# Performance work log

Measured on AMD Instinct MI355X. Metric: run time of the kernel, lower is better.

Reference implementation:

```python
import jax, jax.numpy as jnp
import numpy as np

B, H, W, C = 32, 64, 64, 256


def setup_inputs() -> dict:
    key = jax.random.key(0)
    ks = jax.random.split(key, 4)
    scale = 1.0 / np.sqrt(C)
    return {
        "x": jax.random.normal(ks[0], (B, H, W, C), dtype=jnp.float32),
        "wq": jax.random.normal(ks[1], (C, C), dtype=jnp.float32) * scale,
        "bq": jnp.zeros((C,), dtype=jnp.float32),
        "wk": jax.random.normal(ks[2], (C, C), dtype=jnp.float32) * scale,
        "bk": jnp.zeros((C,), dtype=jnp.float32),
        "wv": jax.random.normal(ks[3], (C, C), dtype=jnp.float32) * scale,
        "bv": jnp.zeros((C,), dtype=jnp.float32),
    }


def reference(x, wq, bq, wk, bk, wv, bv):
    # 1x1 convs == per-pixel dense projections
    q = jnp.einsum('bhwc,cf->bhwf', x, wq) + bq
    k = jnp.einsum('bhwc,cf->bhwf', x, wk) + bk
    v = jnp.einsum('bhwc,cf->bhwf', x, wv) + bv
    # tf.matmul(key, query, transpose_b=True): batch dims (b,h), contract over c
    attn = jnp.einsum('bhwc,bhvc->bhwv', k, q)  # [B,H,W,W], NO 1/sqrt(d) scaling
    attn = jax.nn.softmax(attn, axis=-1)
    out = jnp.einsum('bhwv,bhvc->bhwc', attn, v)  # [B,H,W,C]
    return out * x  # elementwise gate with raw input
```

## Files before the change

### kernel.cpp

```cpp
#include <hip/hip_runtime.h>

#define CD   256
#define WD   64
#define NBH  2048
#define XST  264
#define VST  72
#define SST  68

typedef unsigned short u16;
typedef __attribute__((ext_vector_type(8))) short bfrag_t;
typedef __attribute__((ext_vector_type(4))) float f4_t;

#define MFMA(a, b, c) __builtin_amdgcn_mfma_f32_16x16x32_bf16(a, b, c, 0, 0, 0)

__device__ __forceinline__ u16 f2bf(float f) {
    unsigned u = __float_as_uint(f);
    u += 0x7fffu + ((u >> 16) & 1u);
    return (u16)(u >> 16);
}
__device__ __forceinline__ float bf2f(u16 h) {
    return __uint_as_float(((unsigned)h) << 16);
}

__global__ __launch_bounds__(256) void prep_all(
    const float* __restrict__ wq, const float* __restrict__ wk,
    const float* __restrict__ wv, const float* __restrict__ bk,
    u16* __restrict__ Mthi, u16* __restrict__ Mtlo,
    u16* __restrict__ Wvthi, float* __restrict__ wqbk)
{
    __shared__ float smem[12336];
    const int t = threadIdx.x;
    const int b = blockIdx.x;

    if (b < 128) {
        float* swq = smem;
        float* swk = smem + 16 * 257;
        const int dt = b >> 3;
        const int ct = b & 7;
        #pragma unroll
        for (int n = 0; n < 16; ++n) {
            int idx = n * 256 + t;
            int d = idx >> 8, f = idx & 255;
            swq[d * 257 + f] = wq[(dt * 16 + d) * CD + f];
        }
        #pragma unroll
        for (int n = 0; n < 32; ++n) {
            int idx = n * 256 + t;
            int c = idx >> 8, f = idx & 255;
            swk[c * 257 + f] = wk[(ct * 32 + c) * CD + f];
        }
        __syncthreads();
        const int d = t & 15, c0 = (t >> 4) * 2;
        #pragma unroll
        for (int cc = 0; cc < 2; ++cc) {
            const float* kr = &swk[(c0 + cc) * 257];
            const float* qr = &swq[d * 257];
            float acc = 0.f;
            #pragma unroll 8
            for (int f = 0; f < CD; ++f) acc = fmaf(kr[f], qr[f], acc);
            u16 h = f2bf(acc);
            int off = (dt * 16 + d) * CD + ct * 32 + c0 + cc;
            Mthi[off] = h;
            Mtlo[off] = f2bf(acc - bf2f(h));
        }
    } else if (b < 144) {
        float* tile = smem;
        const int bb = b - 128;
        const int bc = bb >> 2, bd = bb & 3;
        #pragma unroll
        for (int n = 0; n < 16; ++n) {
            int idx = n * 256 + t;
            int c = idx >> 6, d = idx & 63;
            tile[c * 65 + d] = wv[(bc * 64 + c) * CD + bd * 64 + d];
        }
        __syncthreads();
        #pragma unroll
        for (int n = 0; n < 16; ++n) {
            int idx = n * 256 + t;
            int d = idx >> 6, c = idx & 63;
            Wvthi[(bd * 64 + d) * CD + bc * 64 + c] = f2bf(tile[c * 65 + d]);
        }
    } else {
        float* sbk = smem;
        if (t < CD) sbk[t] = bk[t];
        __syncthreads();
        const int c = (b - 144) * 16 + (t >> 4), part = t & 15;
        const float* wr = wq + c * CD + part * 16;
        const float* br = sbk + part * 16;
        float a = 0.f;
        #pragma unroll
        for (int j = 0; j < 16; ++j) a = fmaf(wr[j], br[j], a);
        a += __shfl_xor(a, 1);
        a += __shfl_xor(a, 2);
        a += __shfl_xor(a, 4);
        a += __shfl_xor(a, 8);
        if (part == 0) wqbk[c] = a;
    }
}

extern __shared__ char smem_raw[];

__global__ __launch_bounds__(1024, 4) void attn_kernel(
    const float* __restrict__ x,
    const u16* __restrict__ Mthi, const u16* __restrict__ Mtlo,
    const u16* __restrict__ Wvthi, const float* __restrict__ wqbk,
    const float* __restrict__ bv, float* __restrict__ out)
{
    u16* sXhi = (u16*)smem_raw;
    u16* sXlo = sXhi + WD * XST;
    u16* sThi = sXlo + WD * XST;
    u16* sTlo = sThi + WD * XST;
    u16* sVt  = sThi;
    float* sS  = (float*)(sTlo + WD * XST);
    float* sxb = sS + WD * SST;
    float* sbv = sxb + WD;

    const int t = threadIdx.x;
    const int wave = t >> 6, lane = t & 63;
    const int lane15 = lane & 15, quad = lane >> 4;
    const int bh = blockIdx.x;
    const float* __restrict__ xblk = x + (size_t)bh * (WD * CD);
    float* __restrict__ oblk = out + (size_t)bh * (WD * CD);

    if (t < CD) sbv[t] = bv[t];
    {
        const float4* xv4 = (const float4*)xblk;
        #pragma unroll
        for (int n = 0; n < 4; ++n) {
            int idx = n * 1024 + t;
            float4 v = xv4[idx];
            int i = idx >> 6;
            int c = (idx & 63) << 2;
            ushort4 h4, l4;
            h4.x = f2bf(v.x); l4.x = f2bf(v.x - bf2f(h4.x));
            h4.y = f2bf(v.y); l4.y = f2bf(v.y - bf2f(h4.y));
            h4.z = f2bf(v.z); l4.z = f2bf(v.z - bf2f(h4.z));
            h4.w = f2bf(v.w); l4.w = f2bf(v.w - bf2f(h4.w));
            *(ushort4*)&sXhi[i * XST + c] = h4;
            *(ushort4*)&sXlo[i * XST + c] = l4;
        }
    }
    {
        const int row = t >> 4, part = t & 15;
        const float* xr = xblk + row * CD + part * 16;
        const float* br = wqbk + part * 16;
        float a = 0.f;
        #pragma unroll
        for (int i = 0; i < 4; ++i) {
            float4 xv = *(const float4*)&xr[i * 4];
            float4 bvv = *(const float4*)&br[i * 4];
            a = fmaf(xv.x, bvv.x, a); a = fmaf(xv.y, bvv.y, a);
            a = fmaf(xv.z, bvv.z, a); a = fmaf(xv.w, bvv.w, a);
        }
        a += __shfl_xor(a, 1);
        a += __shfl_xor(a, 2);
        a += __shfl_xor(a, 4);
        a += __shfl_xor(a, 8);
        if (part == 0) sxb[row] = a;
    }
    __syncthreads();

    {
        f4_t acc[4];
        const f4_t z = {0.f, 0.f, 0.f, 0.f};
        #pragma unroll
        for (int a = 0; a < 4; ++a) acc[a] = z;

        const int drow = wave * 16 + lane15;
        const u16* mh = Mthi + drow * CD + quad * 8;
        const u16* ml = Mtlo + drow * CD + quad * 8;
        bfrag_t Ah[8], Al[8];
        #pragma unroll
        for (int kk = 0; kk < 8; ++kk) {
            Ah[kk] = *(const bfrag_t*)(mh + kk * 32);
            Al[kk] = *(const bfrag_t*)(ml + kk * 32);
        }
        #pragma unroll
        for (int kk = 0; kk < 8; ++kk) {
            const int k0 = kk * 32 + quad * 8;
            bfrag_t Bh[4], Bl[4];
            #pragma unroll
            for (int nt = 0; nt < 4; ++nt) {
                const int xo = (nt * 16 + lane15) * XST + k0;
                Bh[nt] = *(const bfrag_t*)(sXhi + xo);
                Bl[nt] = *(const bfrag_t*)(sXlo + xo);
            }
            #pragma unroll
            for (int nt = 0; nt < 4; ++nt) {
                acc[nt] = MFMA(Ah[kk], Bh[nt], acc[nt]);
                acc[nt] = MFMA(Ah[kk], Bl[nt], acc[nt]);
                acc[nt] = MFMA(Al[kk], Bh[nt], acc[nt]);
            }
        }
        #pragma unroll
        for (int nt = 0; nt < 4; ++nt) {
            const int i  = nt * 16 + lane15;
            const int d0 = wave * 16 + quad * 4;
            ushort4 h4, l4;
            float f;
            f = acc[nt][0]; h4.x = f2bf(f); l4.x = f2bf(f - bf2f(h4.x));
            f = acc[nt][1]; h4.y = f2bf(f); l4.y = f2bf(f - bf2f(h4.y));
            f = acc[nt][2]; h4.z = f2bf(f); l4.z = f2bf(f - bf2f(h4.z));
            f = acc[nt][3]; h4.w = f2bf(f); l4.w = f2bf(f - bf2f(h4.w));
            *(ushort4*)&sThi[i * XST + d0] = h4;
            *(ushort4*)&sTlo[i * XST + d0] = l4;
        }
    }
    __syncthreads();

    {
        const f4_t z = {0.f, 0.f, 0.f, 0.f};
        f4_t a0 = z, a1 = z, a2 = z;
        const int m0 = (wave >> 2) * 16;
        const int n0 = (wave & 3) * 16;
        #pragma unroll
        for (int kk = 0; kk < 8; ++kk) {
            const int k0 = kk * 32 + quad * 8;
            const int to = (m0 + lane15) * XST + k0;
            const int xo = (n0 + lane15) * XST + k0;
            bfrag_t Th = *(const bfrag_t*)(sThi + to);
            bfrag_t Tl = *(const bfrag_t*)(sTlo + to);
            bfrag_t Xh = *(const bfrag_t*)(sXhi + xo);
            bfrag_t Xl = *(const bfrag_t*)(sXlo + xo);
            a0 = MFMA(Th, Xh, a0);
            a1 = MFMA(Th, Xl, a1);
            a2 = MFMA(Tl, Xh, a2);
        }
        const int v = n0 + lane15;
        const float xbv = sxb[v];
        #pragma unroll
        for (int r = 0; r < 4; ++r) {
            const int wtok = m0 + quad * 4 + r;
            sS[wtok * SST + v] = a0[r] + a1[r] + a2[r] + xbv;
        }
    }
    __syncthreads();

    {
        f4_t acc[4];
        const f4_t z = {0.f, 0.f, 0.f, 0.f};
        #pragma unroll
        for (int a = 0; a < 4; ++a) acc[a] = z;

        const int drow = wave * 16 + lane15;
        const u16* wvp = Wvthi + drow * CD + quad * 8;
        bfrag_t Av[8];
        #pragma unroll
        for (int kk = 0; kk < 8; ++kk)
            Av[kk] = *(const bfrag_t*)(wvp + kk * 32);
        #pragma unroll
        for (int kk = 0; kk < 8; ++kk) {
            const int k0 = kk * 32 + quad * 8;
            #pragma unroll
            for (int nt = 0; nt < 4; ++nt) {
                bfrag_t Bf = *(const bfrag_t*)(sXhi + (nt * 16 + lane15) * XST + k0);
                acc[nt] = MFMA(Av[kk], Bf, acc[nt]);
            }
        }
        #pragma unroll
        for (int nt = 0; nt < 4; ++nt) {
            const int j = nt * 16 + lane15;
            #pragma unroll
            for (int r = 0; r < 4; ++r) {
                const int d = wave * 16 + quad * 4 + r;
                sVt[d * VST + j] = f2bf(acc[nt][r] + sbv[d]);
            }
        }
    }
    {
        const int row = t >> 4, part = t & 15;
        float* srow = &sS[row * SST + part * 4];
        float e[4];
        float mx = fmaxf(fmaxf(srow[0], srow[1]), fmaxf(srow[2], srow[3]));
        mx = fmaxf(mx, __shfl_xor(mx, 1));
        mx = fmaxf(mx, __shfl_xor(mx, 2));
        mx = fmaxf(mx, __shfl_xor(mx, 4));
        mx = fmaxf(mx, __shfl_xor(mx, 8));
        float sum = 0.f;
        #pragma unroll
        for (int u = 0; u < 4; ++u) { e[u] = __expf(srow[u] - mx); sum += e[u]; }
        sum += __shfl_xor(sum, 1);
        sum += __shfl_xor(sum, 2);
        sum += __shfl_xor(sum, 4);
        sum += __shfl_xor(sum, 8);
        float inv = 1.0f / sum;
        #pragma unroll
        for (int u = 0; u < 4; ++u) srow[u] = e[u] * inv;
    }
    __syncthreads();

    {
        f4_t acc[4];
        const f4_t z = {0.f, 0.f, 0.f, 0.f};
        #pragma unroll
        for (int a = 0; a < 4; ++a) acc[a] = z;

        const int m0 = (wave & 3) * 16;
        const int nbase = (wave >> 2) * 64;
        #pragma unroll
        for (int kk = 0; kk < 2; ++kk) {
            const int k0 = kk * 32 + quad * 8;
            const float* p = &sS[(m0 + lane15) * SST + k0];
            f4_t p0 = *(const f4_t*)p;
            f4_t p1 = *(const f4_t*)(p + 4);
            bfrag_t Af;
            Af[0] = (short)f2bf(p0[0]); Af[1] = (short)f2bf(p0[1]);
            Af[2] = (short)f2bf(p0[2]); Af[3] = (short)f2bf(p0[3]);
            Af[4] = (short)f2bf(p1[0]); Af[5] = (short)f2bf(p1[1]);
            Af[6] = (short)f2bf(p1[2]); Af[7] = (short)f2bf(p1[3]);
            #pragma unroll
            for (int nt = 0; nt < 4; ++nt) {
                bfrag_t Bf = *(const bfrag_t*)(sVt + (nbase + nt * 16 + lane15) * VST + k0);
                acc[nt] = MFMA(Af, Bf, acc[nt]);
            }
        }
        #pragma unroll
        for (int nt = 0; nt < 4; ++nt) {
            const int d = nbase + nt * 16 + lane15;
            #pragma unroll
            for (int r = 0; r < 4; ++r) {
                const int wtok = m0 + quad * 4 + r;
                float g = xblk[wtok * CD + d];
                oblk[wtok * CD + d] = acc[nt][r] * g;
            }
        }
    }
}

extern "C" void kernel_launch(void* const* d_in, const int* in_sizes, int n_in,
                              void* d_out, int out_size, void* d_ws, size_t ws_size,
                              hipStream_t stream) {
    const float* x  = (const float*)d_in[0];
    const float* wq = (const float*)d_in[1];
    const float* wk = (const float*)d_in[3];
    const float* bk = (const float*)d_in[4];
    const float* wv = (const float*)d_in[5];
    const float* bv = (const float*)d_in[6];
    float* out = (float*)d_out;

    char* ws = (char*)d_ws;
    u16* Mthi   = (u16*)ws;
    u16* Mtlo   = (u16*)(ws + (128 << 10));
    u16* Wvthi  = (u16*)(ws + (256 << 10));
    float* wqbk = (float*)(ws + (384 << 10));

    prep_all<<<160, 256, 0, stream>>>(wq, wk, wv, bk, Mthi, Mtlo, Wvthi, wqbk);

    const size_t lds = (size_t)(4 * WD * XST * sizeof(u16)) +
                       (WD * SST + WD + CD) * sizeof(float);
    hipFuncSetAttribute((const void*)attn_kernel,
                        hipFuncAttributeMaxDynamicSharedMemorySize, (int)lds);
    attn_kernel<<<NBH, 1024, lds, stream>>>(x, Mthi, Mtlo, Wvthi, wqbk, bv, out);
}
```

Before: 374.3 us.

## Make attention kernel persistent with prefetch of next block's input

Launches a fixed grid of 256 blocks that each loop over eight (b,h) slices instead of one block per slice. The next slice's x is loaded from global into registers during the final PV stage, then split into bf16 hi/lo in LDS after a barrier, so load latency overlaps with compute. The x·(wq·bk) bias term and the output gate now read x back from the LDS hi+lo split instead of global memory, removing redundant global reads at slight precision cost. Only one block per CU with 1024 threads, which may reduce latency hiding compared to multiple resident blocks.

```diff
diff --git a/kernel.cpp b/kernel.cpp
--- a/kernel.cpp
+++ b/kernel.cpp
@@ -3,6 +3,8 @@
 #define CD   256
 #define WD   64
 #define NBH  2048
+#define GRID 256
+#define ITER (NBH / GRID)
 #define XST  264
 #define VST  72
 #define SST  68
@@ -118,12 +120,11 @@
     const int t = threadIdx.x;
     const int wave = t >> 6, lane = t & 63;
     const int lane15 = lane & 15, quad = lane >> 4;
-    const int bh = blockIdx.x;
-    const float* __restrict__ xblk = x + (size_t)bh * (WD * CD);
-    float* __restrict__ oblk = out + (size_t)bh * (WD * CD);
 
     if (t < CD) sbv[t] = bv[t];
+
     {
+        const float* __restrict__ xblk = x + (size_t)blockIdx.x * (WD * CD);
         const float4* xv4 = (const float4*)xblk;
         #pragma unroll
         for (int n = 0; n < 4; ++n) {
@@ -140,190 +141,227 @@
             *(ushort4*)&sXlo[i * XST + c] = l4;
         }
     }
-    {
-        const int row = t >> 4, part = t & 15;
-        const float* xr = xblk + row * CD + part * 16;
-        const float* br = wqbk + part * 16;
-        float a = 0.f;
-        #pragma unroll
-        for (int i = 0; i < 4; ++i) {
-            float4 xv = *(const float4*)&xr[i * 4];
-            float4 bvv = *(const float4*)&br[i * 4];
-            a = fmaf(xv.x, bvv.x, a); a = fmaf(xv.y, bvv.y, a);
-            a = fmaf(xv.z, bvv.z, a); a = fmaf(xv.w, bvv.w, a);
-        }
-        a += __shfl_xor(a, 1);
-        a += __shfl_xor(a, 2);
-        a += __shfl_xor(a, 4);
-        a += __shfl_xor(a, 8);
-        if (part == 0) sxb[row] = a;
-    }
     __syncthreads();
 
-    {
-        f4_t acc[4];
-        const f4_t z = {0.f, 0.f, 0.f, 0.f};
-        #pragma unroll
-        for (int a = 0; a < 4; ++a) acc[a] = z;
-
-        const int drow = wave * 16 + lane15;
-        const u16* mh = Mthi + drow * CD + quad * 8;
-        const u16* ml = Mtlo + drow * CD + quad * 8;
-        bfrag_t Ah[8], Al[8];
-        #pragma unroll
-        for (int kk = 0; kk < 8; ++kk) {
-            Ah[kk] = *(const bfrag_t*)(mh + kk * 32);
-            Al[kk] = *(const bfrag_t*)(ml + kk * 32);
-        }
-        #pragma unroll
-        for (int kk = 0; kk < 8; ++kk) {
-            const int k0 = kk * 32 + quad * 8;
-            bfrag_t Bh[4], Bl[4];
+    for (int it = 0; it < ITER; ++it) {
+        const int bh = blockIdx.x + (it << 8);
+        float* __restrict__ oblk = out + (size_t)bh * (WD * CD);
+        const float* __restrict__ xnext = x + (size_t)(bh + GRID) * (WD * CD);
+        const bool hasnext = (it + 1 < ITER);
+
+        {
+            const int row = t >> 4, part = t & 15;
+            const u16* xh = &sXhi[row * XST + part * 16];
+            const u16* xl = &sXlo[row * XST + part * 16];
+            bfrag_t h0 = *(const bfrag_t*)xh;
+            bfrag_t h1 = *(const bfrag_t*)(xh + 8);
+            bfrag_t l0 = *(const bfrag_t*)xl;
+            bfrag_t l1 = *(const bfrag_t*)(xl + 8);
+            const float* br = wqbk + part * 16;
+            float a = 0.f;
+            #pragma unroll
+            for (int j = 0; j < 8; ++j) {
+                a = fmaf(bf2f((u16)h0[j]) + bf2f((u16)l0[j]), br[j], a);
+                a = fmaf(bf2f((u16)h1[j]) + bf2f((u16)l1[j]), br[j + 8], a);
+            }
+            a += __shfl_xor(a, 1);
+            a += __shfl_xor(a, 2);
+            a += __shfl_xor(a, 4);
+            a += __shfl_xor(a, 8);
+            if (part == 0) sxb[row] = a;
+
+            f4_t acc[4];
+            const f4_t z = {0.f, 0.f, 0.f, 0.f};
+            #pragma unroll
+            for (int aa = 0; aa < 4; ++aa) acc[aa] = z;
+
+            const int drow = wave * 16 + lane15;
+            const u16* mh = Mthi + drow * CD + quad * 8;
+            const u16* ml = Mtlo + drow * CD + quad * 8;
+            bfrag_t Ah[8], Al[8];
+            #pragma unroll
+            for (int kk = 0; kk < 8; ++kk) {
+                Ah[kk] = *(const bfrag_t*)(mh + kk * 32);
+                Al[kk] = *(const bfrag_t*)(ml + kk * 32);
+            }
+            #pragma unroll
+            for (int kk = 0; kk < 8; ++kk) {
+                const int k0 = kk * 32 + quad * 8;
+                bfrag_t Bh[4], Bl[4];
+                #pragma unroll
+                for (int nt = 0; nt < 4; ++nt) {
+                    const int xo = (nt * 16 + lane15) * XST + k0;
+                    Bh[nt] = *(const bfrag_t*)(sXhi + xo);
+                    Bl[nt] = *(const bfrag_t*)(sXlo + xo);
+                }
+                #pragma unroll
+                for (int nt = 0; nt < 4; ++nt) {
+                    acc[nt] = MFMA(Ah[kk], Bh[nt], acc[nt]);
+                    acc[nt] = MFMA(Ah[kk], Bl[nt], acc[nt]);
+                    acc[nt] = MFMA(Al[kk], Bh[nt], acc[nt]);
+                }
+            }
             #pragma unroll
             for (int nt = 0; nt < 4; ++nt) {
-                const int xo = (nt * 16 + lane15) * XST + k0;
-                Bh[nt] = *(const bfrag_t*)(sXhi + xo);
-                Bl[nt] = *(const bfrag_t*)(sXlo + xo);
-            }
-            #pragma unroll
-            for (int nt = 0; nt < 4; ++nt) {
-                acc[nt] = MFMA(Ah[kk], Bh[nt], acc[nt]);
-                acc[nt] = MFMA(Ah[kk], Bl[nt], acc[nt]);
-                acc[nt] = MFMA(Al[kk], Bh[nt], acc[nt]);
-            }
-        }
-        #pragma unroll
-        for (int nt = 0; nt < 4; ++nt) {
-            const int i  = nt * 16 + lane15;
-            const int d0 = wave * 16 + quad * 4;
-            ushort4 h4, l4;
-            float f;
-            f = acc[nt][0]; h4.x = f2bf(f); l4.x = f2bf(f - bf2f(h4.x));
-            f = acc[nt][1]; h4.y = f2bf(f); l4.y = f2bf(f - bf2f(h4.y));
-            f = acc[nt][2]; h4.z = f2bf(f); l4.z = f2bf(f - bf2f(h4.z));
-            f = acc[nt][3]; h4.w = f2bf(f); l4.w = f2bf(f - bf2f(h4.w));
-            *(ushort4*)&sThi[i * XST + d0] = h4;
-            *(ushort4*)&sTlo[i * XST + d0] = l4;
-        }
-    }
-    __syncthreads();
-
-    {
-        const f4_t z = {0.f, 0.f, 0.f, 0.f};
-        f4_t a0 = z, a1 = z, a2 = z;
-        const int m0 = (wave >> 2) * 16;
-        const int n0 = (wave & 3) * 16;
-        #pragma unroll
-        for (int kk = 0; kk < 8; ++kk) {
-            const int k0 = kk * 32 + quad * 8;
-            const int to = (m0 + lane15) * XST + k0;
-            const int xo = (n0 + lane15) * XST + k0;
-            bfrag_t Th = *(const bfrag_t*)(sThi + to);
-            bfrag_t Tl = *(const bfrag_t*)(sTlo + to);
-            bfrag_t Xh = *(const bfrag_t*)(sXhi + xo);
-            bfrag_t Xl = *(const bfrag_t*)(sXlo + xo);
-            a0 = MFMA(Th, Xh, a0);
-            a1 = MFMA(Th, Xl, a1);
-            a2 = MFMA(Tl, Xh, a2);
-        }
-        const int v = n0 + lane15;
-        const float xbv = sxb[v];
-        #pragma unroll
-        for (int r = 0; r < 4; ++r) {
-            const int wtok = m0 + quad * 4 + r;
-            sS[wtok * SST + v] = a0[r] + a1[r] + a2[r] + xbv;
-        }
-    }
-    __syncthreads();
-
-    {
-        f4_t acc[4];
-        const f4_t z = {0.f, 0.f, 0.f, 0.f};
-        #pragma unroll
-        for (int a = 0; a < 4; ++a) acc[a] = z;
-
-        const int drow = wave * 16 + lane15;
-        const u16* wvp = Wvthi + drow * CD + quad * 8;
-        bfrag_t Av[8];
-        #pragma unroll
-        for (int kk = 0; kk < 8; ++kk)
-            Av[kk] = *(const bfrag_t*)(wvp + kk * 32);
-        #pragma unroll
-        for (int kk = 0; kk < 8; ++kk) {
-            const int k0 = kk * 32 + quad * 8;
-            #pragma unroll
-            for (int nt = 0; nt < 4; ++nt) {
-                bfrag_t Bf = *(const bfrag_t*)(sXhi + (nt * 16 + lane15) * XST + k0);
-                acc[nt] = MFMA(Av[kk], Bf, acc[nt]);
-            }
-        }
-        #pragma unroll
-        for (int nt = 0; nt < 4; ++nt) {
-            const int j = nt * 16 + lane15;
-            #pragma unroll
-            for (int r = 0; r < 4; ++r) {
-                const int d = wave * 16 + quad * 4 + r;
-                sVt[d * VST + j] = f2bf(acc[nt][r] + sbv[d]);
-            }
-        }
-    }
-    {
-        const int row = t >> 4, part = t & 15;
-        float* srow = &sS[row * SST + part * 4];
-        float e[4];
-        float mx = fmaxf(fmaxf(srow[0], srow[1]), fmaxf(srow[2], srow[3]));
-        mx = fmaxf(mx, __shfl_xor(mx, 1));
-        mx = fmaxf(mx, __shfl_xor(mx, 2));
-        mx = fmaxf(mx, __shfl_xor(mx, 4));
-        mx = fmaxf(mx, __shfl_xor(mx, 8));
-        float sum = 0.f;
-        #pragma unroll
-        for (int u = 0; u < 4; ++u) { e[u] = __expf(srow[u] - mx); sum += e[u]; }
-        sum += __shfl_xor(sum, 1);
-        sum += __shfl_xor(sum, 2);
-        sum += __shfl_xor(sum, 4);
-        sum += __shfl_xor(sum, 8);
-        float inv = 1.0f / sum;
-        #pragma unroll
-        for (int u = 0; u < 4; ++u) srow[u] = e[u] * inv;
-    }
-    __syncthreads();
-
-    {
-        f4_t acc[4];
-        const f4_t z = {0.f, 0.f, 0.f, 0.f};
-        #pragma unroll
-        for (int a = 0; a < 4; ++a) acc[a] = z;
-
-        const int m0 = (wave & 3) * 16;
-        const int nbase = (wave >> 2) * 64;
-        #pragma unroll
-        for (int kk = 0; kk < 2; ++kk) {
-            const int k0 = kk * 32 + quad * 8;
-            const float* p = &sS[(m0 + lane15) * SST + k0];
-            f4_t p0 = *(const f4_t*)p;
-            f4_t p1 = *(const f4_t*)(p + 4);
-            bfrag_t Af;
-            Af[0] = (short)f2bf(p0[0]); Af[1] = (short)f2bf(p0[1]);
-            Af[2] = (short)f2bf(p0[2]); Af[3] = (short)f2bf(p0[3]);
-            Af[4] = (short)f2bf(p1[0]); Af[5] = (short)f2bf(p1[1]);
-            Af[6] = (short)f2bf(p1[2]); Af[7] = (short)f2bf(p1[3]);
-            #pragma unroll
-            for (int nt = 0; nt < 4; ++nt) {
-                bfrag_t Bf = *(const bfrag_t*)(sVt + (nbase + nt * 16 + lane15) * VST + k0);
-                acc[nt] = MFMA(Af, Bf, acc[nt]);
-            }
-        }
-        #pragma unroll
-        for (int nt = 0; nt < 4; ++nt) {
-            const int d = nbase + nt * 16 + lane15;
+                const int i  = nt * 16 + lane15;
+                const int d0 = wave * 16 + quad * 4;
+                ushort4 h4, l4;
+                float f;
+                f = acc[nt][0]; h4.x = f2bf(f); l4.x = f2bf(f - bf2f(h4.x));
+                f = acc[nt][1]; h4.y = f2bf(f); l4.y = f2bf(f - bf2f(h4.y));
+                f = acc[nt][2]; h4.z = f2bf(f); l4.z = f2bf(f - bf2f(h4.z));
+                f = acc[nt][3]; h4.w = f2bf(f); l4.w = f2bf(f - bf2f(h4.w));
+                *(ushort4*)&sThi[i * XST + d0] = h4;
+                *(ushort4*)&sTlo[i * XST + d0] = l4;
+            }
+        }
+        __syncthreads();
+
+        {
+            const f4_t z = {0.f, 0.f, 0.f, 0.f};
+            f4_t a0 = z, a1 = z, a2 = z;
+            const int m0 = (wave >> 2) * 16;
+            const int n0 = (wave & 3) * 16;
+            #pragma unroll
+            for (int kk = 0; kk < 8; ++kk) {
+                const int k0 = kk * 32 + quad * 8;
+                const int to = (m0 + lane15) * XST + k0;
+                const int xo = (n0 + lane15) * XST + k0;
+                bfrag_t Th = *(const bfrag_t*)(sThi + to);
+                bfrag_t Tl = *(const bfrag_t*)(sTlo + to);
+                bfrag_t Xh = *(const bfrag_t*)(sXhi + xo);
+                bfrag_t Xl = *(const bfrag_t*)(sXlo + xo);
+                a0 = MFMA(Th, Xh, a0);
+                a1 = MFMA(Th, Xl, a1);
+                a2 = MFMA(Tl, Xh, a2);
+            }
+            const int v = n0 + lane15;
+            const float xbv = sxb[v];
             #pragma unroll
             for (int r = 0; r < 4; ++r) {
                 const int wtok = m0 + quad * 4 + r;
-                float g = xblk[wtok * CD + d];
-                oblk[wtok * CD + d] = acc[nt][r] * g;
-            }
-        }
+                sS[wtok * SST + v] = a0[r] + a1[r] + a2[r] + xbv;
+            }
+        }
+        __syncthreads();
+
+        {
+            f4_t acc[4];
+            const f4_t z = {0.f, 0.f, 0.f, 0.f};
+            #pragma unroll
+            for (int aa = 0; aa < 4; ++aa) acc[aa] = z;
+
+            const int drow = wave * 16 + lane15;
+            const u16* wvp = Wvthi + drow * CD + quad * 8;
+            bfrag_t Av[8];
+            #pragma unroll
+            for (int kk = 0; kk < 8; ++kk)
+                Av[kk] = *(const bfrag_t*)(wvp + kk * 32);
+            #pragma unroll
+            for (int kk = 0; kk < 8; ++kk) {
+                const int k0 = kk * 32 + quad * 8;
+                #pragma unroll
+                for (int nt = 0; nt < 4; ++nt) {
+                    bfrag_t Bf = *(const bfrag_t*)(sXhi + (nt * 16 + lane15) * XST + k0);
+                    acc[nt] = MFMA(Av[kk], Bf, acc[nt]);
+                }
+            }
+            #pragma unroll
+            for (int nt = 0; nt < 4; ++nt) {
+                const int j = nt * 16 + lane15;
+                #pragma unroll
+                for (int r = 0; r < 4; ++r) {
+                    const int d = wave * 16 + quad * 4 + r;
+                    sVt[d * VST + j] = f2bf(acc[nt][r] + sbv[d]);
+                }
+            }
+        }
+        {
+            const int row = t >> 4, part = t & 15;
+            float* srow = &sS[row * SST + part * 4];
+            float e[4];
+            float mx = fmaxf(fmaxf(srow[0], srow[1]), fmaxf(srow[2], srow[3]));
+            mx = fmaxf(mx, __shfl_xor(mx, 1));
+            mx = fmaxf(mx, __shfl_xor(mx, 2));
+            mx = fmaxf(mx, __shfl_xor(mx, 4));
+            mx = fmaxf(mx, __shfl_xor(mx, 8));
+            float sum = 0.f;
+            #pragma unroll
+            for (int u = 0; u < 4; ++u) { e[u] = __expf(srow[u] - mx); sum += e[u]; }
+            sum += __shfl_xor(sum, 1);
+            sum += __shfl_xor(sum, 2);
+            sum += __shfl_xor(sum, 4);
+            sum += __shfl_xor(sum, 8);
+            float inv = 1.0f / sum;
+            #pragma unroll
+            for (int u = 0; u < 4; ++u) srow[u] = e[u] * inv;
+        }
+        __syncthreads();
+
+        float4 xv[4];
+        {
+            if (hasnext) {
+                const float4* xnv4 = (const float4*)xnext;
+                #pragma unroll
+                for (int n = 0; n < 4; ++n) xv[n] = xnv4[n * 1024 + t];
+            }
+
+            f4_t acc[4];
+            const f4_t z = {0.f, 0.f, 0.f, 0.f};
+            #pragma unroll
+            for (int aa = 0; aa < 4; ++aa) acc[aa] = z;
+
+            const int m0 = (wave & 3) * 16;
+            const int nbase = (wave >> 2) * 64;
+            #pragma unroll
+            for (int kk = 0; kk < 2; ++kk) {
+                const int k0 = kk * 32 + quad * 8;
+                const float* p = &sS[(m0 + lane15) * SST + k0];
+                f4_t p0 = *(const f4_t*)p;
+                f4_t p1 = *(const f4_t*)(p + 4);
+                bfrag_t Af;
+                Af[0] = (short)f2bf(p0[0]); Af[1] = (short)f2bf(p0[1]);
+                Af[2] = (short)f2bf(p0[2]); Af[3] = (short)f2bf(p0[3]);
+                Af[4] = (short)f2bf(p1[0]); Af[5] = (short)f2bf(p1[1]);
+                Af[6] = (short)f2bf(p1[2]); Af[7] = (short)f2bf(p1[3]);
+                #pragma unroll
+                for (int nt = 0; nt < 4; ++nt) {
+                    bfrag_t Bf = *(const bfrag_t*)(sVt + (nbase + nt * 16 + lane15) * VST + k0);
+                    acc[nt] = MFMA(Af, Bf, acc[nt]);
+                }
+            }
+
+            #pragma unroll
+            for (int nt = 0; nt < 4; ++nt) {
+                const int d = nbase + nt * 16 + lane15;
+                #pragma unroll
+                for (int r = 0; r < 4; ++r) {
+                    const int wtok = m0 + quad * 4 + r;
+                    const int go = wtok * XST + d;
+                    float g = bf2f(sXhi[go]) + bf2f(sXlo[go]);
+                    oblk[wtok * CD + d] = acc[nt][r] * g;
+                }
+            }
+        }
+        __syncthreads();
+
+        if (hasnext) {
+            #pragma unroll
+            for (int n = 0; n < 4; ++n) {
+                int idx = n * 1024 + t;
+                int i = idx >> 6;
+                int c = (idx & 63) << 2;
+                float4 v = xv[n];
+                ushort4 h4, l4;
+                h4.x = f2bf(v.x); l4.x = f2bf(v.x - bf2f(h4.x));
+                h4.y = f2bf(v.y); l4.y = f2bf(v.y - bf2f(h4.y));
+                h4.z = f2bf(v.z); l4.z = f2bf(v.z - bf2f(h4.z));
+                h4.w = f2bf(v.w); l4.w = f2bf(v.w - bf2f(h4.w));
+                *(ushort4*)&sXhi[i * XST + c] = h4;
+                *(ushort4*)&sXlo[i * XST + c] = l4;
+            }
+        }
+        __syncthreads();
     }
 }
 
@@ -350,5 +388,5 @@
                        (WD * SST + WD + CD) * sizeof(float);
     hipFuncSetAttribute((const void*)attn_kernel,
                         hipFuncAttributeMaxDynamicSharedMemorySize, (int)lds);
-    attn_kernel<<<NBH, 1024, lds, stream>>>(x, Mthi, Mtlo, Wvthi, wqbk, bv, out);
-}
+    attn_kernel<<<GRID, 1024, lds, stream>>>(x, Mthi, Mtlo, Wvthi, wqbk, bv, out);
+}
```

Measured after the change: 424.9 us. +13.5%, slower.
